# Kernel tuning notes

Measured on AMD Instinct MI355X. Metric: run time of the kernel, lower is better.

## Reference

```python
import jax, jax.numpy as jnp
import numpy as np

N = 100000      # nodes
E = 1600000     # edges (before self-loops)
F_IN = 128
H = 4           # heads, layer 1
C = 32          # hidden_size (per-head channels)
G = 256         # graphs in batch
NEG_SLOPE = 0.2 # PyG GATConv default


def setup_inputs() -> dict:
    key = jax.random.key(0)
    ks = jax.random.split(key, 12)
    x = jax.random.normal(ks[0], (N, F_IN), jnp.float32)
    edge_index = jax.random.randint(ks[1], (2, E), 0, N, dtype=jnp.int64)
    batch = jnp.sort(jax.random.randint(ks[2], (N,), 0, G, dtype=jnp.int64))
    s = lambda f: np.float32(1.0 / np.sqrt(f))
    W1 = jax.random.normal(ks[3], (F_IN, H * C), jnp.float32) * s(F_IN)
    att_src1 = jax.random.normal(ks[4], (H, C), jnp.float32) * 0.1
    att_dst1 = jax.random.normal(ks[5], (H, C), jnp.float32) * 0.1
    b1 = jnp.zeros((H * C,), jnp.float32)
    W2 = jax.random.normal(ks[6], (H * C, C), jnp.float32) * s(H * C)
    att_src2 = jax.random.normal(ks[7], (1, C), jnp.float32) * 0.1
    att_dst2 = jax.random.normal(ks[8], (1, C), jnp.float32) * 0.1
    b2 = jnp.zeros((C,), jnp.float32)
    Wfc = jax.random.normal(ks[9], (C, 1), jnp.float32) * s(C)
    bfc = jnp.zeros((1,), jnp.float32)
    return {"x": x, "edge_index": edge_index, "batch": batch,
            "W1": W1, "att_src1": att_src1, "att_dst1": att_dst1, "b1": b1,
            "W2": W2, "att_src2": att_src2, "att_dst2": att_dst2, "b2": b2,
            "Wfc": Wfc, "bfc": bfc}


def gat_conv(x, src, dst, W, att_s, att_d, b, heads, ch):
    """PyG GATConv (concat=True): linear, per-head additive attention,
    segment softmax over destination nodes, scatter-add aggregation."""
    n = x.shape[0]
    h = (x @ W).reshape(n, heads, ch)                         # [N,H,C]
    a_s = jnp.einsum('nhc,hc->nh', h, att_s)                  # [N,H]
    a_d = jnp.einsum('nhc,hc->nh', h, att_d)                  # [N,H]
    e = jax.nn.leaky_relu(a_s[src] + a_d[dst], NEG_SLOPE)     # [E,H]
    m = jax.ops.segment_max(e, dst, num_segments=n)           # stable softmax
    e = jnp.exp(e - m[dst])
    denom = jax.ops.segment_sum(e, dst, num_segments=n)
    alpha = e / denom[dst]                                    # [E,H]
    out = jax.ops.segment_sum(h[src] * alpha[:, :, None], dst, num_segments=n)
    return out.reshape(n, heads * ch) + b


def reference(x, edge_index, batch, W1, att_src1, att_dst1, b1,
              W2, att_src2, att_dst2, b2, Wfc, bfc):
    n = x.shape[0]
    loops = jnp.arange(n, dtype=edge_index.dtype)             # PyG add_self_loops=True
    src = jnp.concatenate([edge_index[0], loops])
    dst = jnp.concatenate([edge_index[1], loops])
    h = jax.nn.relu(gat_conv(x, src, dst, W1, att_src1, att_dst1, b1, H, C))
    h = jax.nn.relu(gat_conv(h, src, dst, W2, att_src2, att_dst2, b2, 1, C))
    # global_mean_pool over ragged graph segments
    sums = jax.ops.segment_sum(h, batch, num_segments=G)      # [G,C]
    cnts = jax.ops.segment_sum(jnp.ones((n,), h.dtype), batch, num_segments=G)
    pooled = sums / jnp.maximum(cnts, 1.0)[:, None]
    return (pooled @ Wfc + bfc).squeeze(-1)                   # [G]
```

## Files before the change

kernel.cpp:

```cpp
#include <hip/hip_runtime.h>
#include <cmath>

#define NEG_SLOPE 0.2f
#define DPB 128
#define EPB 2048

typedef unsigned int uint32;
typedef unsigned short ushort16;
typedef unsigned char uchar8;
typedef __attribute__((ext_vector_type(8))) short bf16x8;
typedef __attribute__((ext_vector_type(4))) float f32x4;
typedef __attribute__((ext_vector_type(2))) float f32x2;

__device__ __forceinline__ ushort16 f2bf(float x) {
    uint32 b = __float_as_uint(x);
    b += 0x7FFFu + ((b >> 16) & 1u);
    return (ushort16)(b >> 16);
}
__device__ __forceinline__ float bf2f_lo(uint32 u) { return __uint_as_float(u << 16); }
__device__ __forceinline__ float bf2f_hi(uint32 u) { return __uint_as_float(u & 0xFFFF0000u); }

__global__ void prep_B1(const float* __restrict__ W1, const float* __restrict__ atts,
                        const float* __restrict__ attd, ushort16* __restrict__ Bt) {
    int idx = blockIdx.x * 256 + threadIdx.x;
    if (idx >= 144 * 128) return;
    int n = idx >> 7, k = idx & 127;
    float v = 0.f;
    if (n < 128) v = W1[k * 128 + n];
    else if (n < 132) { int h = n - 128; for (int c = 0; c < 32; c++) v += W1[k*128 + h*32 + c] * atts[h*32 + c]; }
    else if (n < 136) { int h = n - 132; for (int c = 0; c < 32; c++) v += W1[k*128 + h*32 + c] * attd[h*32 + c]; }
    Bt[idx] = f2bf(v);
}
__global__ void prep_B2(const float* __restrict__ W2, const float* __restrict__ atts,
                        const float* __restrict__ attd, ushort16* __restrict__ Bt) {
    int idx = blockIdx.x * 256 + threadIdx.x;
    if (idx >= 48 * 128) return;
    int n = idx >> 7, k = idx & 127;
    float v = 0.f;
    if (n < 32) v = W2[k * 32 + n];
    else if (n == 32) { for (int c = 0; c < 32; c++) v += W2[k*32 + c] * atts[c]; }
    else if (n == 33) { for (int c = 0; c < 32; c++) v += W2[k*32 + c] * attd[c]; }
    Bt[idx] = f2bf(v);
}

template<int NT, int NH, bool XBF, bool OUT8>
__global__ __launch_bounds__(256) void gemm_mfma(
    const void* __restrict__ Xv, const ushort16* __restrict__ Bt,
    void* __restrict__ Houtv, float* __restrict__ asd, int M)
{
    constexpr int HT = NT - 1;
    constexpr int KP = 136;
    __shared__ ushort16 Bl[NT * 16 * KP];
    const int t = threadIdx.x;
    for (int i = t; i < NT * 16 * 32; i += 256) {
        int n = i >> 5, k4 = i & 31;
        uint2 v = *(const uint2*)&Bt[n * 128 + k4 * 4];
        *(uint2*)&Bl[n * KP + k4 * 4] = v;
    }
    __syncthreads();
    const int wave = t >> 6, lane = t & 63;
    const int lrow = lane & 15, lgrp = lane >> 4;
    const int ntiles = (M + 127) >> 7;
    const float* Xf = (const float*)Xv;
    const ushort16* Xb = (const ushort16*)Xv;

    for (int tile = blockIdx.x; tile < ntiles; tile += gridDim.x) {
        const int rbase = tile * 128 + wave * 32;
        f32x4 acc[2][NT];
        #pragma unroll
        for (int rs = 0; rs < 2; rs++)
            #pragma unroll
            for (int n = 0; n < NT; n++) acc[rs][n] = (f32x4){0.f, 0.f, 0.f, 0.f};

        for (int kk = 0; kk < 4; kk++) {
            bf16x8 bf[NT];
            #pragma unroll
            for (int n = 0; n < NT; n++)
                bf[n] = *(const bf16x8*)&Bl[(n * 16 + lrow) * KP + kk * 32 + lgrp * 8];
            #pragma unroll
            for (int rs = 0; rs < 2; rs++) {
                int row = rbase + rs * 16 + lrow;
                int rowc = row < M ? row : M - 1;
                bf16x8 af;
                if constexpr (XBF) {
                    af = *(const bf16x8*)&Xb[(long)rowc * 128 + kk * 32 + lgrp * 8];
                } else {
                    const float* xp = Xf + (long)rowc * 128 + kk * 32 + lgrp * 8;
                    float4 f0 = *(const float4*)xp;
                    float4 f1 = *(const float4*)(xp + 4);
                    union { uint32 u[4]; bf16x8 v; } pk;
                    pk.u[0] = (uint32)f2bf(f0.x) | ((uint32)f2bf(f0.y) << 16);
                    pk.u[1] = (uint32)f2bf(f0.z) | ((uint32)f2bf(f0.w) << 16);
                    pk.u[2] = (uint32)f2bf(f1.x) | ((uint32)f2bf(f1.y) << 16);
                    pk.u[3] = (uint32)f2bf(f1.z) | ((uint32)f2bf(f1.w) << 16);
                    af = pk.v;
                }
                #pragma unroll
                for (int n = 0; n < NT; n++)
                    acc[rs][n] = __builtin_amdgcn_mfma_f32_16x16x32_bf16(af, bf[n], acc[rs][n], 0, 0, 0);
            }
        }
        #pragma unroll
        for (int rs = 0; rs < 2; rs++) {
            #pragma unroll
            for (int r = 0; r < 4; r++) {
                const int row = rbase + rs * 16 + lgrp * 4 + r;
                if (row < M) {
                    if constexpr (OUT8) {
                        uchar8* H8 = (uchar8*)Houtv;
                        #pragma unroll
                        for (int n = 0; n < HT; n++) {
                            int pk = __builtin_amdgcn_cvt_pk_fp8_f32(acc[rs][n][r], 0.f, 0, false);
                            H8[(long)row * (HT * 16) + n * 16 + lrow] = (uchar8)pk;
                        }
                    } else {
                        ushort16* Hh = (ushort16*)Houtv;
                        #pragma unroll
                        for (int n = 0; n < HT; n++)
                            Hh[(long)row * (HT * 16) + n * 16 + lrow] = f2bf(acc[rs][n][r]);
                    }
                    if (lrow < 2 * NH)
                        asd[(long)row * (2 * NH) + lrow] = acc[rs][NT - 1][r];
                }
            }
        }
    }
}


__global__ __launch_bounds__(256) void buck_hist_k(
    const int* __restrict__ ei, int E, int Etot,
    int* __restrict__ cnt_bb, int NBUK_, int NBLK_)
{
    __shared__ int hist[1024];
    const int b = blockIdx.x, t = threadIdx.x;
    for (int i = t; i < NBUK_; i += 256) hist[i] = 0;
    __syncthreads();
    const int e0 = b * EPB;
    for (int i = t; i < EPB; i += 256) {
        int e = e0 + i;
        if (e < Etot) {
            int d = (e < E) ? ei[E + e] : (e - E);
            atomicAdd(&hist[d >> 7], 1);
        }
    }
    __syncthreads();
    for (int i = t; i < NBUK_; i += 256) cnt_bb[(size_t)i * NBLK_ + b] = hist[i];
}

__global__ __launch_bounds__(256) void buck_scan_row_k(
    int* __restrict__ cnt_bb, int* __restrict__ rowTot, int NBLK_)
{
    __shared__ int tmp[256];
    const int k = blockIdx.x, t = threadIdx.x;
    int* row = cnt_bb + (size_t)k * NBLK_;
    const int base = t * 4;
    int v[4]; int s = 0;
    #pragma unroll
    for (int j = 0; j < 4; j++) { v[j] = (base + j < NBLK_) ? row[base + j] : 0; s += v[j]; }
    tmp[t] = s; __syncthreads();
    for (int off = 1; off < 256; off <<= 1) {
        int x = (t >= off) ? tmp[t - off] : 0;
        __syncthreads();
        tmp[t] += x;
        __syncthreads();
    }
    int run = tmp[t] - s;
    if (t == 255) rowTot[k] = tmp[255];
    #pragma unroll
    for (int j = 0; j < 4; j++) { if (base + j < NBLK_) row[base + j] = run; run += v[j]; }
}

__global__ __launch_bounds__(256) void buck_base_k(
    const int* __restrict__ rowTot, int* __restrict__ bucketBase, int NBUK_)
{
    __shared__ int tmp[256];
    const int t = threadIdx.x;
    const int base = t * 4;
    int v[4]; int s = 0;
    #pragma unroll
    for (int j = 0; j < 4; j++) {
        v[j] = (base + j < NBUK_) ? ((rowTot[base + j] + 3 * DPB + 7) & ~7) : 0;
        s += v[j];
    }
    tmp[t] = s; __syncthreads();
    for (int off = 1; off < 256; off <<= 1) {
        int x = (t >= off) ? tmp[t - off] : 0;
        __syncthreads();
        tmp[t] += x;
        __syncthreads();
    }
    int run = tmp[t] - s;
    #pragma unroll
    for (int j = 0; j < 4; j++) { if (base + j < NBUK_) bucketBase[base + j] = run; run += v[j]; }
}

__global__ __launch_bounds__(256) void buck_scatter_k(
    const int* __restrict__ ei, int E, int Etot,
    const int* __restrict__ cnt_bb, const int* __restrict__ bucketBase,
    uint32* __restrict__ be, int NBUK_, int NBLK_)
{
    __shared__ int cur[1024];
    const int b = blockIdx.x, t = threadIdx.x;
    for (int i = t; i < NBUK_; i += 256)
        cur[i] = bucketBase[i] + cnt_bb[(size_t)i * NBLK_ + b];
    __syncthreads();
    const int e0 = b * EPB;
    for (int i = t; i < EPB; i += 256) {
        int e = e0 + i;
        if (e < Etot) {
            int srcv, d;
            if (e < E) { srcv = ei[e]; d = ei[E + e]; } else { srcv = d = e - E; }
            int slot = atomicAdd(&cur[d >> 7], 1);
            be[slot] = (uint32)srcv | ((uint32)(d & (DPB - 1)) << 20);
        }
    }
}

__global__ __launch_bounds__(256) void buck_finalize_k(
    const uint32* __restrict__ be, const int* __restrict__ rowTot,
    const int* __restrict__ bucketBase,
    int* __restrict__ csr, int* __restrict__ indptr, int* __restrict__ count, int N_)
{
    __shared__ int lhist[DPB];
    __shared__ int lptr[DPB];
    __shared__ int lcur[DPB];
    __shared__ int stmp[DPB];
    __shared__ int img[6144];
    __shared__ int paddedTotS;
    const int k = blockIdx.x, t = threadIdx.x;
    const int baseG = bucketBase[k];
    const int Mk = rowTot[k];
    if (t < DPB) lhist[t] = 0;
    __syncthreads();
    for (int i = t; i < Mk; i += 256) atomicAdd(&lhist[be[baseG + i] >> 20], 1);
    __syncthreads();
    int myp = (t < DPB) ? ((lhist[t] + 3) & ~3) : 0;
    if (t < DPB) stmp[t] = myp;
    __syncthreads();
    for (int off = 1; off < DPB; off <<= 1) {
        int x = (t < DPB && t >= off) ? stmp[t - off] : 0;
        __syncthreads();
        if (t < DPB) stmp[t] += x;
        __syncthreads();
    }
    if (t < DPB) { lptr[t] = stmp[t] - myp; lcur[t] = stmp[t] - myp; }
    if (t == DPB - 1) paddedTotS = stmp[t];
    __syncthreads();
    const int paddedTot = paddedTotS < 6144 ? paddedTotS : 6144;
    for (int i = t; i < paddedTot; i += 256) img[i] = 0;
    if (t < DPB) {
        int d = k * DPB + t;
        if (d < N_) { count[d] = lhist[t]; indptr[d] = baseG + lptr[t]; }
    }
    __syncthreads();
    for (int i = t; i < Mk; i += 256) {
        uint32 pk = be[baseG + i];
        int slot = atomicAdd(&lcur[pk >> 20], 1);
        if (slot < 6144) img[slot] = (int)(pk & 0xFFFFFu);
    }
    __syncthreads();
    for (int i = t; i < paddedTot; i += 256) csr[baseG + i] = img[i];
}

__global__ __launch_bounds__(256) void edge_p_k(
    const int* __restrict__ csr, const int* __restrict__ indptr, const int* __restrict__ count,
    const float* __restrict__ asd, ushort16* __restrict__ p1h, int N, int EP)
{
    int wave = threadIdx.x >> 6, lane = threadIdx.x & 63;
    int dst = blockIdx.x * 4 + wave;
    if (dst >= N) return;
    const int start = indptr[dst], cnt = count[dst];
    const int cntp = (cnt + 3) & ~3;
    const float4 ad = *(const float4*)&asd[(long)dst * 8 + 4];
    for (int k = lane; k < cntp; k += 64) {
        ushort16 r0 = 0, r1 = 0, r2 = 0, r3 = 0;
        if (k < cnt) {
            int s = csr[start + k];
            float4 as = *(const float4*)&asd[(long)s * 8];
            float e0 = as.x + ad.x, e1 = as.y + ad.y, e2 = as.z + ad.z, e3 = as.w + ad.w;
            e0 = e0 >= 0.f ? e0 : NEG_SLOPE * e0;
            e1 = e1 >= 0.f ? e1 : NEG_SLOPE * e1;
            e2 = e2 >= 0.f ? e2 : NEG_SLOPE * e2;
            e3 = e3 >= 0.f ? e3 : NEG_SLOPE * e3;
            r0 = f2bf(__expf(e0)); r1 = f2bf(__expf(e1));
            r2 = f2bf(__expf(e2)); r3 = f2bf(__expf(e3));
        }
        const int pos = start + k;
        p1h[pos] = r0;
        p1h[EP + pos] = r1;
        p1h[2 * EP + pos] = r2;
        p1h[3 * EP + pos] = r3;
    }
}

__global__ __launch_bounds__(256) void edge_p2_k(
    const int* __restrict__ csr, const int* __restrict__ indptr, const int* __restrict__ count,
    const float* __restrict__ asd2, ushort16* __restrict__ p2, int N)
{
    int wave = threadIdx.x >> 6, lane = threadIdx.x & 63;
    int dst = blockIdx.x * 4 + wave;
    if (dst >= N) return;
    const int start = indptr[dst], cnt = count[dst];
    const int cntp = (cnt + 3) & ~3;
    const float ad = asd2[(long)dst * 2 + 1];
    for (int k = lane; k < cntp; k += 64) {
        ushort16 r = 0;
        if (k < cnt) {
            float el = asd2[(long)csr[start + k] * 2] + ad;
            el = el >= 0.f ? el : NEG_SLOPE * el;
            r = f2bf(__expf(el));
        }
        p2[start + k] = r;
    }
}

__global__ __launch_bounds__(256) void agg_flash_h4(
    const int* __restrict__ csr, const ushort16* __restrict__ p1h,
    const int* __restrict__ indptr, const int* __restrict__ count,
    const uchar8* __restrict__ H8, const float* __restrict__ b1,
    uint32* __restrict__ Out, int N, int EP)
{
    int wave = threadIdx.x >> 6, lane = threadIdx.x & 63;
    int dst = blockIdx.x * 4 + wave;
    if (dst >= N) return;
    const int head = lane >> 4;
    const int ch2 = lane * 2;
    const int start = indptr[dst], cnt = count[dst];
    const int cntp = (cnt + 3) & ~3;
    const ushort16* pp = p1h + (size_t)head * EP + start;
    float s = 0.f, a0 = 0.f, a1 = 0.f;
    int k = 0;
    for (; k + 8 <= cntp; k += 8) {
        const int4 svA = *(const int4*)&csr[start + k];
        const int4 svB = *(const int4*)&csr[start + k + 4];
        const uint2 pwA = *(const uint2*)&pp[k];
        const uint2 pwB = *(const uint2*)&pp[k + 4];
        const uint32 u0 = *(const ushort16*)&H8[(long)svA.x * 128 + ch2];
        const uint32 u1 = *(const ushort16*)&H8[(long)svA.y * 128 + ch2];
        const uint32 u2 = *(const ushort16*)&H8[(long)svA.z * 128 + ch2];
        const uint32 u3 = *(const ushort16*)&H8[(long)svA.w * 128 + ch2];
        const uint32 u4 = *(const ushort16*)&H8[(long)svB.x * 128 + ch2];
        const uint32 u5 = *(const ushort16*)&H8[(long)svB.y * 128 + ch2];
        const uint32 u6 = *(const ushort16*)&H8[(long)svB.z * 128 + ch2];
        const uint32 u7 = *(const ushort16*)&H8[(long)svB.w * 128 + ch2];
        const f32x2 h0 = __builtin_amdgcn_cvt_pk_f32_fp8((int)u0, false);
        const f32x2 h1 = __builtin_amdgcn_cvt_pk_f32_fp8((int)u1, false);
        const f32x2 h2 = __builtin_amdgcn_cvt_pk_f32_fp8((int)u2, false);
        const f32x2 h3 = __builtin_amdgcn_cvt_pk_f32_fp8((int)u3, false);
        const f32x2 h4 = __builtin_amdgcn_cvt_pk_f32_fp8((int)u4, false);
        const f32x2 h5 = __builtin_amdgcn_cvt_pk_f32_fp8((int)u5, false);
        const f32x2 h6 = __builtin_amdgcn_cvt_pk_f32_fp8((int)u6, false);
        const f32x2 h7 = __builtin_amdgcn_cvt_pk_f32_fp8((int)u7, false);
        const float p0 = bf2f_lo(pwA.x), p1v = bf2f_hi(pwA.x);
        const float p2v = bf2f_lo(pwA.y), p3v = bf2f_hi(pwA.y);
        const float p4v = bf2f_lo(pwB.x), p5v = bf2f_hi(pwB.x);
        const float p6v = bf2f_lo(pwB.y), p7v = bf2f_hi(pwB.y);
        s += ((p0 + p1v) + (p2v + p3v)) + ((p4v + p5v) + (p6v + p7v));
        a0 += p0 * h0[0];  a1 += p0 * h0[1];
        a0 += p1v * h1[0]; a1 += p1v * h1[1];
        a0 += p2v * h2[0]; a1 += p2v * h2[1];
        a0 += p3v * h3[0]; a1 += p3v * h3[1];
        a0 += p4v * h4[0]; a1 += p4v * h4[1];
        a0 += p5v * h5[0]; a1 += p5v * h5[1];
        a0 += p6v * h6[0]; a1 += p6v * h6[1];
        a0 += p7v * h7[0]; a1 += p7v * h7[1];
    }
    if (k < cntp) {
        const int4 sv = *(const int4*)&csr[start + k];
        const uint2 pw = *(const uint2*)&pp[k];
        const uint32 u0 = *(const ushort16*)&H8[(long)sv.x * 128 + ch2];
        const uint32 u1 = *(const ushort16*)&H8[(long)sv.y * 128 + ch2];
        const uint32 u2 = *(const ushort16*)&H8[(long)sv.z * 128 + ch2];
        const uint32 u3 = *(const ushort16*)&H8[(long)sv.w * 128 + ch2];
        const f32x2 h0 = __builtin_amdgcn_cvt_pk_f32_fp8((int)u0, false);
        const f32x2 h1 = __builtin_amdgcn_cvt_pk_f32_fp8((int)u1, false);
        const f32x2 h2 = __builtin_amdgcn_cvt_pk_f32_fp8((int)u2, false);
        const f32x2 h3 = __builtin_amdgcn_cvt_pk_f32_fp8((int)u3, false);
        const float p0 = bf2f_lo(pw.x), p1v = bf2f_hi(pw.x);
        const float p2v = bf2f_lo(pw.y), p3v = bf2f_hi(pw.y);
        s += (p0 + p1v) + (p2v + p3v);
        a0 += p0 * h0[0];  a1 += p0 * h0[1];
        a0 += p1v * h1[0]; a1 += p1v * h1[1];
        a0 += p2v * h2[0]; a1 += p2v * h2[1];
        a0 += p3v * h3[0]; a1 += p3v * h3[1];
    }
    const float inv = 1.f / s;
    const float2 bb = *(const float2*)&b1[ch2];
    float o0 = fmaxf(a0 * inv + bb.x, 0.f);
    float o1 = fmaxf(a1 * inv + bb.y, 0.f);
    Out[(long)dst * 64 + lane] = (uint32)f2bf(o0) | ((uint32)f2bf(o1) << 16);
}

__global__ __launch_bounds__(256) void agg_flash_h1(
    const int* __restrict__ csr, const ushort16* __restrict__ p2,
    const int* __restrict__ indptr, const int* __restrict__ count,
    const uchar8* __restrict__ H8, float* __restrict__ Out, int N)
{
    int wave = threadIdx.x >> 6, lane = threadIdx.x & 63;
    int dst = blockIdx.x * 4 + wave;
    if (dst >= N) return;
    const int c2 = lane & 15, grp = lane >> 4;
    const int start = indptr[dst];
    const int cntp = (count[dst] + 3) & ~3;
    float s = 0.f, a0 = 0.f, a1 = 0.f;
    for (int k = grp * 4; k < cntp; k += 16) {
        const int4  sv = *(const int4*)&csr[start + k];
        const uint2 pv = *(const uint2*)&p2[start + k];
        const uint32 u0 = *(const ushort16*)&H8[(long)sv.x * 32 + c2 * 2];
        const uint32 u1 = *(const ushort16*)&H8[(long)sv.y * 32 + c2 * 2];
        const uint32 u2 = *(const ushort16*)&H8[(long)sv.z * 32 + c2 * 2];
        const uint32 u3 = *(const ushort16*)&H8[(long)sv.w * 32 + c2 * 2];
        const f32x2 h0 = __builtin_amdgcn_cvt_pk_f32_fp8((int)u0, false);
        const f32x2 h1 = __builtin_amdgcn_cvt_pk_f32_fp8((int)u1, false);
        const f32x2 h2 = __builtin_amdgcn_cvt_pk_f32_fp8((int)u2, false);
        const f32x2 h3 = __builtin_amdgcn_cvt_pk_f32_fp8((int)u3, false);
        float q0 = bf2f_lo(pv.x), q1 = bf2f_hi(pv.x);
        float q2 = bf2f_lo(pv.y), q3 = bf2f_hi(pv.y);
        s += (q0 + q1) + (q2 + q3);
        a0 += q0 * h0[0]; a1 += q0 * h0[1];
        a0 += q1 * h1[0]; a1 += q1 * h1[1];
        a0 += q2 * h2[0]; a1 += q2 * h2[1];
        a0 += q3 * h3[0]; a1 += q3 * h3[1];
    }
    s  += __shfl_xor(s, 16, 64);  s  += __shfl_xor(s, 32, 64);
    a0 += __shfl_xor(a0, 16, 64); a0 += __shfl_xor(a0, 32, 64);
    a1 += __shfl_xor(a1, 16, 64); a1 += __shfl_xor(a1, 32, 64);
    if (grp == 0) {
        const float inv = 1.f / s;
        float2 o; o.x = a0 * inv; o.y = a1 * inv;
        *(float2*)&Out[(long)dst * 32 + c2 * 2] = o;
    }
}

__global__ __launch_bounds__(256) void pool_fc_kernel(
    const float* __restrict__ Agg2, const float* __restrict__ b2,
    const int* __restrict__ batch,
    const float* __restrict__ Wfc, const float* __restrict__ bfc,
    float* __restrict__ out, int N)
{
    __shared__ float part[8][32];
    const int g = blockIdx.x;
    const int t = threadIdx.x;
    const int c = t & 31, grp = t >> 5;

    int lo = 0, hi = N;
    while (lo < hi) { int mid = (lo + hi) >> 1; if (batch[mid] < g) lo = mid + 1; else hi = mid; }
    const int start = lo;
    hi = N;
    while (lo < hi) { int mid = (lo + hi) >> 1; if (batch[mid] <= g) lo = mid + 1; else hi = mid; }
    const int end = lo;

    const float bc = b2[c];
    float acc = 0.f;
    for (int i = start + grp; i < end; i += 8)
        acc += fmaxf(Agg2[(long)i * 32 + c] + bc, 0.f);
    part[grp][c] = acc;
    __syncthreads();
    if (t < 32) {
        float s = 0.f;
        #pragma unroll
        for (int r = 0; r < 8; r++) s += part[r][c];
        const float cnt = fmaxf((float)(end - start), 1.f);
        float v = (s / cnt) * Wfc[c];
        #pragma unroll
        for (int m = 16; m >= 1; m >>= 1) v += __shfl_xor(v, m, 64);
        if (c == 0) out[g] = v + bfc[0];
    }
}

extern "C" void kernel_launch(void* const* d_in, const int* in_sizes, int n_in,
                              void* d_out, int out_size, void* d_ws, size_t ws_size,
                              hipStream_t stream)
{
    const float* x     = (const float*)d_in[0];
    const int*   ei    = (const int*)d_in[1];
    const int*   batch = (const int*)d_in[2];
    const float* W1    = (const float*)d_in[3];
    const float* atts1 = (const float*)d_in[4];
    const float* attd1 = (const float*)d_in[5];
    const float* b1    = (const float*)d_in[6];
    const float* W2    = (const float*)d_in[7];
    const float* atts2 = (const float*)d_in[8];
    const float* attd2 = (const float*)d_in[9];
    const float* b2    = (const float*)d_in[10];
    const float* Wfc   = (const float*)d_in[11];
    const float* bfc   = (const float*)d_in[12];
    float* out = (float*)d_out;

    const int N = in_sizes[0] / 128;
    const int E = in_sizes[1] / 2;
    const int Etot = E + N;
    const int G = out_size;
    const int NBUK = (N + DPB - 1) / DPB;
    const int NBLK = (Etot + EPB - 1) / EPB;
    const int CSRCAP = (Etot + NBUK * (3 * DPB + 8) + 7) & ~7;

    float* w = (float*)d_ws;
    uchar8* h1   = (uchar8*)w; w += (size_t)N * 32;
    uchar8* h2   = (uchar8*)w; w += (size_t)N * 8;
    uint32* agg1 = (uint32*)w; w += (size_t)N * 64;
    float* agg2 = w; w += (size_t)N * 32;
    float* asd1 = w; w += (size_t)N * 8;
    float* asd2 = w; w += (size_t)N * 2;
    ushort16* Bt1 = (ushort16*)w; w += (144 * 128) / 2;
    ushort16* Bt2 = (ushort16*)w; w += (48 * 128) / 2;
    int* count  = (int*)w; w += N;
    int* indptr = (int*)w; w += N;
    int* cnt_bb = (int*)w; w += (size_t)NBUK * NBLK;
    int* rowTot = (int*)w; w += NBUK;
    int* bucketBase = (int*)w; w += NBUK;
    uint32* be  = (uint32*)w; w += CSRCAP;
    int* csr    = (int*)w; w += CSRCAP;
    ushort16* p1h = (ushort16*)w; w += (size_t)CSRCAP * 2;
    ushort16* p2  = (ushort16*)w; w += CSRCAP / 2;

    prep_B1<<<(144 * 128 + 255) / 256, 256, 0, stream>>>(W1, atts1, attd1, Bt1);
    prep_B2<<<(48 * 128 + 255) / 256, 256, 0, stream>>>(W2, atts2, attd2, Bt2);

    gemm_mfma<9, 4, false, true><<<512, 256, 0, stream>>>(x, Bt1, h1, asd1, N);

    buck_hist_k<<<NBLK, 256, 0, stream>>>(ei, E, Etot, cnt_bb, NBUK, NBLK);
    buck_scan_row_k<<<NBUK, 256, 0, stream>>>(cnt_bb, rowTot, NBLK);
    buck_base_k<<<1, 256, 0, stream>>>(rowTot, bucketBase, NBUK);
    buck_scatter_k<<<NBLK, 256, 0, stream>>>(ei, E, Etot, cnt_bb, bucketBase, be, NBUK, NBLK);
    buck_finalize_k<<<NBUK, 256, 0, stream>>>(be, rowTot, bucketBase, csr, indptr, count, N);

    edge_p_k<<<(N + 3) / 4, 256, 0, stream>>>(csr, indptr, count, asd1, p1h, N, CSRCAP);
    agg_flash_h4<<<(N + 3) / 4, 256, 0, stream>>>(csr, p1h, indptr, count, h1, b1, agg1, N, CSRCAP);

    gemm_mfma<3, 1, true, true><<<512, 256, 0, stream>>>(agg1, Bt2, h2, asd2, N);
    edge_p2_k<<<(N + 3) / 4, 256, 0, stream>>>(csr, indptr, count, asd2, p2, N);
    agg_flash_h1<<<(N + 3) / 4, 256, 0, stream>>>(csr, p2, indptr, count, h2, agg2, N);

    pool_fc_kernel<<<G, 256, 0, stream>>>(agg2, b2, batch, Wfc, bfc, out, N);
}
```

Baseline: 246.9 us.

## Use 32-bit shift-or addressing in gathers, enlarge edge blocks, size GEMM grids by tiles

```diff
diff --git a/kernel.cpp b/kernel.cpp
--- a/kernel.cpp
+++ b/kernel.cpp
@@ -3,7 +3,7 @@
 
 #define NEG_SLOPE 0.2f
 #define DPB 128
-#define EPB 2048
+#define EPB 4096
 
 typedef unsigned int uint32;
 typedef unsigned short ushort16;
@@ -127,7 +127,6 @@
     }
 }
 
-
 __global__ __launch_bounds__(256) void buck_hist_k(
     const int* __restrict__ ei, int E, int Etot,
     int* __restrict__ cnt_bb, int NBUK_, int NBLK_)
@@ -270,14 +269,15 @@
     int wave = threadIdx.x >> 6, lane = threadIdx.x & 63;
     int dst = blockIdx.x * 4 + wave;
     if (dst >= N) return;
+    const char* asdb = (const char*)asd;
     const int start = indptr[dst], cnt = count[dst];
     const int cntp = (cnt + 3) & ~3;
-    const float4 ad = *(const float4*)&asd[(long)dst * 8 + 4];
+    const float4 ad = *(const float4*)(asdb + (((uint32)dst << 5) | 16u));
     for (int k = lane; k < cntp; k += 64) {
         ushort16 r0 = 0, r1 = 0, r2 = 0, r3 = 0;
         if (k < cnt) {
-            int s = csr[start + k];
-            float4 as = *(const float4*)&asd[(long)s * 8];
+            uint32 s = (uint32)csr[start + k];
+            float4 as = *(const float4*)(asdb + (s << 5));
             float e0 = as.x + ad.x, e1 = as.y + ad.y, e2 = as.z + ad.z, e3 = as.w + ad.w;
             e0 = e0 >= 0.f ? e0 : NEG_SLOPE * e0;
             e1 = e1 >= 0.f ? e1 : NEG_SLOPE * e1;
@@ -301,13 +301,15 @@
     int wave = threadIdx.x >> 6, lane = threadIdx.x & 63;
     int dst = blockIdx.x * 4 + wave;
     if (dst >= N) return;
+    const char* asdb = (const char*)asd2;
     const int start = indptr[dst], cnt = count[dst];
     const int cntp = (cnt + 3) & ~3;
-    const float ad = asd2[(long)dst * 2 + 1];
+    const float ad = *(const float*)(asdb + (((uint32)dst << 3) | 4u));
     for (int k = lane; k < cntp; k += 64) {
         ushort16 r = 0;
         if (k < cnt) {
-            float el = asd2[(long)csr[start + k] * 2] + ad;
+            uint32 s = (uint32)csr[start + k];
+            float el = *(const float*)(asdb + (s << 3)) + ad;
             el = el >= 0.f ? el : NEG_SLOPE * el;
             r = f2bf(__expf(el));
         }
@@ -324,8 +326,9 @@
     int wave = threadIdx.x >> 6, lane = threadIdx.x & 63;
     int dst = blockIdx.x * 4 + wave;
     if (dst >= N) return;
+    const char* Hb = (const char*)H8;
     const int head = lane >> 4;
-    const int ch2 = lane * 2;
+    const uint32 ch2 = (uint32)(lane * 2);
     const int start = indptr[dst], cnt = count[dst];
     const int cntp = (cnt + 3) & ~3;
     const ushort16* pp = p1h + (size_t)head * EP + start;
@@ -336,14 +339,14 @@
         const int4 svB = *(const int4*)&csr[start + k + 4];
         const uint2 pwA = *(const uint2*)&pp[k];
         const uint2 pwB = *(const uint2*)&pp[k + 4];
-        const uint32 u0 = *(const ushort16*)&H8[(long)svA.x * 128 + ch2];
-        const uint32 u1 = *(const ushort16*)&H8[(long)svA.y * 128 + ch2];
-        const uint32 u2 = *(const ushort16*)&H8[(long)svA.z * 128 + ch2];
-        const uint32 u3 = *(const ushort16*)&H8[(long)svA.w * 128 + ch2];
-        const uint32 u4 = *(const ushort16*)&H8[(long)svB.x * 128 + ch2];
-        const uint32 u5 = *(const ushort16*)&H8[(long)svB.y * 128 + ch2];
-        const uint32 u6 = *(const ushort16*)&H8[(long)svB.z * 128 + ch2];
-        const uint32 u7 = *(const ushort16*)&H8[(long)svB.w * 128 + ch2];
+        const uint32 u0 = *(const ushort16*)(Hb + (((uint32)svA.x << 7) | ch2));
+        const uint32 u1 = *(const ushort16*)(Hb + (((uint32)svA.y << 7) | ch2));
+        const uint32 u2 = *(const ushort16*)(Hb + (((uint32)svA.z << 7) | ch2));
+        const uint32 u3 = *(const ushort16*)(Hb + (((uint32)svA.w << 7) | ch2));
+        const uint32 u4 = *(const ushort16*)(Hb + (((uint32)svB.x << 7) | ch2));
+        const uint32 u5 = *(const ushort16*)(Hb + (((uint32)svB.y << 7) | ch2));
+        const uint32 u6 = *(const ushort16*)(Hb + (((uint32)svB.z << 7) | ch2));
+        const uint32 u7 = *(const ushort16*)(Hb + (((uint32)svB.w << 7) | ch2));
         const f32x2 h0 = __builtin_amdgcn_cvt_pk_f32_fp8((int)u0, false);
         const f32x2 h1 = __builtin_amdgcn_cvt_pk_f32_fp8((int)u1, false);
         const f32x2 h2 = __builtin_amdgcn_cvt_pk_f32_fp8((int)u2, false);
@@ -369,10 +372,10 @@
     if (k < cntp) {
         const int4 sv = *(const int4*)&csr[start + k];
         const uint2 pw = *(const uint2*)&pp[k];
-        const uint32 u0 = *(const ushort16*)&H8[(long)sv.x * 128 + ch2];
-        const uint32 u1 = *(const ushort16*)&H8[(long)sv.y * 128 + ch2];
-        const uint32 u2 = *(const ushort16*)&H8[(long)sv.z * 128 + ch2];
-        const uint32 u3 = *(const ushort16*)&H8[(long)sv.w * 128 + ch2];
+        const uint32 u0 = *(const ushort16*)(Hb + (((uint32)sv.x << 7) | ch2));
+        const uint32 u1 = *(const ushort16*)(Hb + (((uint32)sv.y << 7) | ch2));
+        const uint32 u2 = *(const ushort16*)(Hb + (((uint32)sv.z << 7) | ch2));
+        const uint32 u3 = *(const ushort16*)(Hb + (((uint32)sv.w << 7) | ch2));
         const f32x2 h0 = __builtin_amdgcn_cvt_pk_f32_fp8((int)u0, false);
         const f32x2 h1 = __builtin_amdgcn_cvt_pk_f32_fp8((int)u1, false);
         const f32x2 h2 = __builtin_amdgcn_cvt_pk_f32_fp8((int)u2, false);
@@ -400,17 +403,19 @@
     int wave = threadIdx.x >> 6, lane = threadIdx.x & 63;
     int dst = blockIdx.x * 4 + wave;
     if (dst >= N) return;
+    const char* Hb = (const char*)H8;
     const int c2 = lane & 15, grp = lane >> 4;
+    const uint32 cb = (uint32)(c2 * 2);
     const int start = indptr[dst];
     const int cntp = (count[dst] + 3) & ~3;
     float s = 0.f, a0 = 0.f, a1 = 0.f;
     for (int k = grp * 4; k < cntp; k += 16) {
         const int4  sv = *(const int4*)&csr[start + k];
         const uint2 pv = *(const uint2*)&p2[start + k];
-        const uint32 u0 = *(const ushort16*)&H8[(long)sv.x * 32 + c2 * 2];
-        const uint32 u1 = *(const ushort16*)&H8[(long)sv.y * 32 + c2 * 2];
-        const uint32 u2 = *(const ushort16*)&H8[(long)sv.z * 32 + c2 * 2];
-        const uint32 u3 = *(const ushort16*)&H8[(long)sv.w * 32 + c2 * 2];
+        const uint32 u0 = *(const ushort16*)(Hb + (((uint32)sv.x << 5) | cb));
+        const uint32 u1 = *(const ushort16*)(Hb + (((uint32)sv.y << 5) | cb));
+        const uint32 u2 = *(const ushort16*)(Hb + (((uint32)sv.z << 5) | cb));
+        const uint32 u3 = *(const ushort16*)(Hb + (((uint32)sv.w << 5) | cb));
         const f32x2 h0 = __builtin_amdgcn_cvt_pk_f32_fp8((int)u0, false);
         const f32x2 h1 = __builtin_amdgcn_cvt_pk_f32_fp8((int)u1, false);
         const f32x2 h2 = __builtin_amdgcn_cvt_pk_f32_fp8((int)u2, false);
@@ -495,6 +500,7 @@
     const int NBUK = (N + DPB - 1) / DPB;
     const int NBLK = (Etot + EPB - 1) / EPB;
     const int CSRCAP = (Etot + NBUK * (3 * DPB + 8) + 7) & ~7;
+    const int ntiles = (N + 127) >> 7;
 
     float* w = (float*)d_ws;
     uchar8* h1   = (uchar8*)w; w += (size_t)N * 32;
@@ -518,7 +524,7 @@
     prep_B1<<<(144 * 128 + 255) / 256, 256, 0, stream>>>(W1, atts1, attd1, Bt1);
     prep_B2<<<(48 * 128 + 255) / 256, 256, 0, stream>>>(W2, atts2, attd2, Bt2);
 
-    gemm_mfma<9, 4, false, true><<<512, 256, 0, stream>>>(x, Bt1, h1, asd1, N);
+    gemm_mfma<9, 4, false, true><<<ntiles, 256, 0, stream>>>(x, Bt1, h1, asd1, N);
 
     buck_hist_k<<<NBLK, 256, 0, stream>>>(ei, E, Etot, cnt_bb, NBUK, NBLK);
     buck_scan_row_k<<<NBUK, 256, 0, stream>>>(cnt_bb, rowTot, NBLK);
@@ -529,7 +535,7 @@
     edge_p_k<<<(N + 3) / 4, 256, 0, stream>>>(csr, indptr, count, asd1, p1h, N, CSRCAP);
     agg_flash_h4<<<(N + 3) / 4, 256, 0, stream>>>(csr, p1h, indptr, count, h1, b1, agg1, N, CSRCAP);
 
-    gemm_mfma<3, 1, true, true><<<512, 256, 0, stream>>>(agg1, Bt2, h2, asd2, N);
+    gemm_mfma<3, 1, true, true><<<ntiles, 256, 0, stream>>>(agg1, Bt2, h2, asd2, N);
     edge_p2_k<<<(N + 3) / 4, 256, 0, stream>>>(csr, indptr, count, asd2, p2, N);
     agg_flash_h1<<<(N + 3) / 4, 256, 0, stream>>>(csr, p2, indptr, count, h2, agg2, N);
 
```

New measurement: 242.2 us. About the same (-1.9%).
